# Kernel tuning notes

Hardware: AMD Instinct MI355X
Metric: run time of the kernel (lower is better)

Reference implementation:

```python
import jax, jax.numpy as jnp
import numpy as np

D_MODEL = 2048
NUM_Q_HEADS = 32
NUM_KV_HEADS = 8
HEAD_DIM = D_MODEL // NUM_Q_HEADS  # 64
NUM_GROUPS = NUM_Q_HEADS // NUM_KV_HEADS  # 4
SCALE = float(np.sqrt(HEAD_DIM))


def setup_inputs() -> dict:
    key = jax.random.key(0)
    ks = jax.random.split(key, 5)
    B, S = 2, 2048
    std = 1.0 / np.sqrt(D_MODEL)
    return {
        "x": jax.random.normal(ks[0], (B, S, D_MODEL), dtype=jnp.float32),
        "W_q": jax.random.normal(ks[1], (D_MODEL, NUM_Q_HEADS * HEAD_DIM), dtype=jnp.float32) * std,
        "W_k": jax.random.normal(ks[2], (D_MODEL, NUM_KV_HEADS * HEAD_DIM), dtype=jnp.float32) * std,
        "W_v": jax.random.normal(ks[3], (D_MODEL, NUM_KV_HEADS * HEAD_DIM), dtype=jnp.float32) * std,
        "W_o": jax.random.normal(ks[4], (D_MODEL, D_MODEL), dtype=jnp.float32) * std,
    }


def reference(x, W_q, W_k, W_v, W_o):
    B, S, _ = x.shape
    # projections; weights stored as (in, out) so y = x @ W
    Q = (x @ W_q).reshape(B, S, NUM_Q_HEADS, HEAD_DIM).transpose(0, 2, 1, 3)   # [B,Hq,S,d]
    K = (x @ W_k).reshape(B, S, NUM_KV_HEADS, HEAD_DIM).transpose(0, 2, 1, 3)  # [B,Hkv,S,d]
    V = (x @ W_v).reshape(B, S, NUM_KV_HEADS, HEAD_DIM).transpose(0, 2, 1, 3)
    # repeat_interleave KV heads across groups (faithful to the original)
    K = jnp.repeat(K, NUM_GROUPS, axis=1)  # [B,Hq,S,d]
    V = jnp.repeat(V, NUM_GROUPS, axis=1)
    scores = jnp.einsum("bhqd,bhkd->bhqk", Q, K) / SCALE  # [B,Hq,S,S]
    attn = jax.nn.softmax(scores, axis=-1)
    out = jnp.einsum("bhqk,bhkd->bhqd", attn, V)  # [B,Hq,S,d]
    out = out.transpose(0, 2, 1, 3).reshape(B, S, D_MODEL)
    return out @ W_o
```

## Files before the change

### kernel.cpp

```cpp
#include <hip/hip_runtime.h>
#include <hip/hip_bf16.h>

#define D_MODEL 2048
#define NQH 32
#define NKVH 8
#define HD 64
#define SEQ 2048
#define BATCH 2
#define MTOT (BATCH * SEQ)

typedef __attribute__((ext_vector_type(8))) short short8;
typedef __attribute__((ext_vector_type(4))) float floatx4;
typedef __attribute__((ext_vector_type(16))) float f32x16;

#define QSCALE 0.18033688011112042f

#if __has_builtin(__builtin_amdgcn_exp2f)
#define EXP2(x) __builtin_amdgcn_exp2f(x)
#else
#define EXP2(x) exp2f(x)
#endif

static __device__ inline unsigned cvtpk(float lo, float hi) {
  unsigned r;
  asm("v_cvt_pk_bf16_f32 %0, %1, %2" : "=v"(r) : "v"(lo), "v"(hi));
  return r;
}
#define PLSWAP(a, b) asm("v_permlane32_swap_b32 %0, %1" : "+v"(a), "+v"(b))

__device__ inline void gload_lds16(const __hip_bfloat16* g, short* lds) {
  __builtin_amdgcn_global_load_lds(
      (const __attribute__((address_space(1))) void*)g,
      (__attribute__((address_space(3))) void*)lds, 16, 0, 0);
}

__global__ __launch_bounds__(256) void convx_k(const float* __restrict__ x,
                                               __hip_bfloat16* __restrict__ xb,
                                               int n4) {
  int i = blockIdx.x * 256 + threadIdx.x;
  int stride = gridDim.x * 256;
  for (; i < n4; i += stride) {
    float4 v = reinterpret_cast<const float4*>(x)[i];
    union { __hip_bfloat16 h[4]; uint2 u; } cv;
    cv.h[0] = __float2bfloat16(v.x);
    cv.h[1] = __float2bfloat16(v.y);
    cv.h[2] = __float2bfloat16(v.z);
    cv.h[3] = __float2bfloat16(v.w);
    reinterpret_cast<uint2*>(xb)[i] = cv.u;
  }
}

__global__ __launch_bounds__(256) void transw_all_k(
    const float* __restrict__ Wq, const float* __restrict__ Wk,
    const float* __restrict__ Wv, const float* __restrict__ Wo,
    __hip_bfloat16* __restrict__ Wqt, __hip_bfloat16* __restrict__ Wkt,
    __hip_bfloat16* __restrict__ Wvt, __hip_bfloat16* __restrict__ Wot) {
  __shared__ float t[32][33];
  const int z = blockIdx.z;
  const int Nd = (z == 1 || z == 2) ? 512 : 2048;
  const int n0 = blockIdx.x * 32;
  if (n0 >= Nd) return;
  const float* W = (z == 0) ? Wq : (z == 1) ? Wk : (z == 2) ? Wv : Wo;
  __hip_bfloat16* Wt = (z == 0) ? Wqt : (z == 1) ? Wkt : (z == 2) ? Wvt : Wot;
  const int Kd = D_MODEL;
  const int k0 = blockIdx.y * 32;
  const int tx = threadIdx.x, ty = threadIdx.y;
#pragma unroll
  for (int j = 0; j < 32; j += 8)
    t[ty + j][tx] = W[(size_t)(k0 + ty + j) * Nd + n0 + tx];
  __syncthreads();
#pragma unroll
  for (int j = 0; j < 32; j += 8)
    Wt[(size_t)(n0 + ty + j) * Kd + k0 + tx] = __float2bfloat16(t[tx][ty + j]);
}

template <int MODE>
__global__ __launch_bounds__(512, 1) void gemm8p_k(
    const __hip_bfloat16* __restrict__ A,
    const __hip_bfloat16* __restrict__ B0,
    const __hip_bfloat16* __restrict__ B1,
    const __hip_bfloat16* __restrict__ B2,
    float* __restrict__ Cf,
    __hip_bfloat16* __restrict__ O0,
    __hip_bfloat16* __restrict__ O1,
    __hip_bfloat16* __restrict__ O2) {
  constexpr int Kd = D_MODEL;
  constexpr int NT = Kd / 64;
  constexpr int NB = (MODE == 0) ? 16 : 24;
  constexpr int NWG = 16 * NB;

  __shared__ short Asb[3][16384];
  __shared__ short Bsb[3][8192];

  const int bid = blockIdx.x;
  const int swz = (bid & 7) * (NWG / 8) + (bid >> 3);
  const int by = swz / NB, bx = swz % NB;
  const int m0 = by * 256, n0 = bx * 128;

  const __hip_bfloat16* Bt;
  if (MODE == 0) {
    Bt = B0 + (size_t)n0 * Kd;
  } else {
    if (n0 < 2048) Bt = B0 + (size_t)n0 * Kd;
    else if (n0 < 2560) Bt = B1 + (size_t)(n0 - 2048) * Kd;
    else Bt = B2 + (size_t)(n0 - 2560) * Kd;
  }
  const __hip_bfloat16* Ab = A + (size_t)m0 * Kd;

  const int tid = threadIdx.x, w = tid >> 6, l = tid & 63;
  const int wm = w >> 1, wn = w & 1;
  const int lc = l & 15, l4 = l >> 4;

  const int srow = w * 8 + (l >> 3);
  const int scc = (l & 7) ^ ((l >> 3) & 7);

#define STAGE_A(L, SB, KT) \
  gload_lds16(Ab + (size_t)((L)*64 + srow) * Kd + (KT) + scc * 8, &Asb[SB][(L)*4096 + w * 512])
#define STAGE_B(L, SB, KT) \
  gload_lds16(Bt + (size_t)((L)*64 + srow) * Kd + (KT) + scc * 8, &Bsb[SB][(L)*4096 + w * 512])

  floatx4 acc[4][4] = {};

  int cx[2];
#pragma unroll
  for (int kk = 0; kk < 2; ++kk) cx[kk] = (((kk * 4 + l4) ^ (lc & 7)) * 8);
  const int abase = (wm * 64 + lc) * 64;
  const int bbase = (wn * 64 + lc) * 64;

  STAGE_A(0, 0, 0); STAGE_A(1, 0, 0); STAGE_A(2, 0, 0); STAGE_A(3, 0, 0);
  STAGE_B(0, 0, 0); STAGE_B(1, 0, 0);
  STAGE_A(0, 1, 64); STAGE_A(1, 1, 64); STAGE_A(2, 1, 64); STAGE_A(3, 1, 64);
  STAGE_B(0, 1, 64); STAGE_B(1, 1, 64);
  asm volatile("s_waitcnt vmcnt(6)" ::: "memory");
  __builtin_amdgcn_s_barrier();

  short8 af[4], bfr[4];

  for (int t = 0; t < NT; ++t) {
    const int rb = t % 3, sb = (t + 2) % 3;
    const int ksrc = ((t + 2) % NT) * 64;
    const short* Ar = Asb[rb];
    const short* Br = Bsb[rb];

#pragma unroll
    for (int mi = 0; mi < 4; ++mi)
      af[mi] = *reinterpret_cast<const short8*>(&Ar[abase + mi * 1024 + cx[0]]);
#pragma unroll
    for (int ni = 0; ni < 4; ++ni)
      bfr[ni] = *reinterpret_cast<const short8*>(&Br[bbase + ni * 1024 + cx[0]]);

    STAGE_A(0, sb, ksrc); STAGE_A(1, sb, ksrc); STAGE_B(0, sb, ksrc);

    __builtin_amdgcn_s_barrier();
    asm volatile("s_waitcnt lgkmcnt(0)" ::: "memory");
    __builtin_amdgcn_sched_barrier(0);
    __builtin_amdgcn_s_setprio(1);
#pragma unroll
    for (int mi = 0; mi < 4; ++mi)
#pragma unroll
      for (int ni = 0; ni < 4; ++ni)
        acc[mi][ni] = __builtin_amdgcn_mfma_f32_16x16x32_bf16(
            af[mi], bfr[ni], acc[mi][ni], 0, 0, 0);
    __builtin_amdgcn_s_setprio(0);
    __builtin_amdgcn_s_barrier();

#pragma unroll
    for (int mi = 0; mi < 4; ++mi)
      af[mi] = *reinterpret_cast<const short8*>(&Ar[abase + mi * 1024 + cx[1]]);
#pragma unroll
    for (int ni = 0; ni < 4; ++ni)
      bfr[ni] = *reinterpret_cast<const short8*>(&Br[bbase + ni * 1024 + cx[1]]);

    STAGE_A(2, sb, ksrc); STAGE_A(3, sb, ksrc); STAGE_B(1, sb, ksrc);

    asm volatile("s_waitcnt vmcnt(6)" ::: "memory");
    __builtin_amdgcn_s_barrier();
    asm volatile("s_waitcnt lgkmcnt(0)" ::: "memory");
    __builtin_amdgcn_sched_barrier(0);
    __builtin_amdgcn_s_setprio(1);
#pragma unroll
    for (int mi = 0; mi < 4; ++mi)
#pragma unroll
      for (int ni = 0; ni < 4; ++ni)
        acc[mi][ni] = __builtin_amdgcn_mfma_f32_16x16x32_bf16(
            af[mi], bfr[ni], acc[mi][ni], 0, 0, 0);
    __builtin_amdgcn_s_setprio(0);
    __builtin_amdgcn_s_barrier();
  }
#undef STAGE_A
#undef STAGE_B

#pragma unroll
  for (int mi = 0; mi < 4; ++mi)
#pragma unroll
    for (int ni = 0; ni < 4; ++ni)
#pragma unroll
      for (int i = 0; i < 4; ++i) {
        int m = m0 + wm * 64 + mi * 16 + l4 * 4 + i;
        int ncol = n0 + wn * 64 + ni * 16 + lc;
        float v = acc[mi][ni][i];
        if (MODE == 0) {
          Cf[(size_t)m * 2048 + ncol] = v;
        } else {
          int bb = m >> 11, s = m & 2047;
          if (ncol < 2048) {
            int hh = ncol >> 6, dd = ncol & 63;
            O0[(((size_t)bb * NQH + hh) * SEQ + s) * HD + dd] = __float2bfloat16(v * QSCALE);
          } else if (ncol < 2560) {
            int c2 = ncol - 2048;
            int hh = c2 >> 6, dd = c2 & 63;
            O1[(((size_t)bb * NKVH + hh) * SEQ + s) * HD + dd] = __float2bfloat16(v);
          } else {
            int c2 = ncol - 2560;
            int hh = c2 >> 6, dd = c2 & 63;
            O2[(((size_t)bb * NKVH + hh) * HD + dd) * SEQ + s] = __float2bfloat16(v);
          }
        }
      }
}

__global__ __launch_bounds__(256, 4) void attn_k(const __hip_bfloat16* __restrict__ Qb,
                                                 const __hip_bfloat16* __restrict__ Kb,
                                                 const __hip_bfloat16* __restrict__ Vtb,
                                                 __hip_bfloat16* __restrict__ Ao) {
  __shared__ short Ks[2][64 * 64];
  __shared__ short Vs[2][64 * 64];
  __shared__ float Ls[4][32];

  const int bid = blockIdx.x;
  const int xcd = bid & 7, j = bid >> 3;
  const int g = xcd * 2 + (j >> 6), wv = j & 63;
  const int b = g >> 3, kh = g & 7;
  const int h = kh * 4 + (wv >> 4), qt = wv & 15;

  const int tid = threadIdx.x, w = tid >> 6, l = tid & 63;
  const int q5 = l & 31, hl = l >> 5;

  const __hip_bfloat16* Qp = Qb + (((size_t)b * NQH + h) * SEQ + qt * 128 + w * 32) * HD;
  const __hip_bfloat16* Kp = Kb + ((size_t)b * NKVH + kh) * SEQ * HD;
  const __hip_bfloat16* Vp = Vtb + ((size_t)b * NKVH + kh) * HD * SEQ;

  short8 qf[4];
#pragma unroll
  for (int ks = 0; ks < 4; ++ks)
    qf[ks] = *reinterpret_cast<const short8*>(Qp + (size_t)q5 * HD + ks * 16 + hl * 8);

  f32x16 acc0 = {}, acc1 = {};
  float lsum = 0.f;

  const int rg = l >> 3;
  const int cc = (l & 7) ^ (rg & 7);
  const __hip_bfloat16* sK = Kp + (size_t)(16 * w + rg) * HD + cc * 8;
  const __hip_bfloat16* sV = Vp + (size_t)(16 * w + rg) * SEQ + cc * 8;

  int fo[4];
#pragma unroll
  for (int jj = 0; jj < 4; ++jj)
    fo[jj] = q5 * 64 + (((jj * 2 + hl) ^ (q5 & 7)) * 8);

  gload_lds16(sK, &Ks[0][1024 * w]);
  gload_lds16(sK + 8 * HD, &Ks[0][1024 * w + 512]);
  gload_lds16(sV, &Vs[0][1024 * w]);
  gload_lds16(sV + 8 * (size_t)SEQ, &Vs[0][1024 * w + 512]);
  sK += 64 * HD;
  sV += 64;
  __syncthreads();

  for (int kb = 0; kb < SEQ / 64; ++kb) {
    const short* Kt = Ks[kb & 1];
    const short* Vt = Vs[kb & 1];

    if (kb + 1 < SEQ / 64) {
      short* Kn = Ks[(kb & 1) ^ 1];
      short* Vn = Vs[(kb & 1) ^ 1];
      gload_lds16(sK, &Kn[1024 * w]);
      gload_lds16(sK + 8 * HD, &Kn[1024 * w + 512]);
      gload_lds16(sV, &Vn[1024 * w]);
      gload_lds16(sV + 8 * (size_t)SEQ, &Vn[1024 * w + 512]);
      sK += 64 * HD;
      sV += 64;
    }

    short8 kf0[4], kf1[4];
#pragma unroll
    for (int ks = 0; ks < 4; ++ks) {
      kf0[ks] = *reinterpret_cast<const short8*>(&Kt[fo[ks]]);
      kf1[ks] = *reinterpret_cast<const short8*>(&Kt[fo[ks] + 2048]);
    }
    f32x16 st0 = {}, st1 = {};
    __builtin_amdgcn_s_setprio(1);
#pragma unroll
    for (int ks = 0; ks < 4; ++ks) {
      st0 = __builtin_amdgcn_mfma_f32_32x32x16_bf16(kf0[ks], qf[ks], st0, 0, 0, 0);
      st1 = __builtin_amdgcn_mfma_f32_32x32x16_bf16(kf1[ks], qf[ks], st1, 0, 0, 0);
    }
    __builtin_amdgcn_s_setprio(0);

    float ps = 0.f;
    unsigned u0[8], u1[8];
#pragma unroll
    for (int jj = 0; jj < 8; ++jj) {
      float e0 = EXP2(st0[2 * jj]), e1 = EXP2(st0[2 * jj + 1]);
      float f0 = EXP2(st1[2 * jj]), f1 = EXP2(st1[2 * jj + 1]);
      ps += (e0 + e1) + (f0 + f1);
      u0[jj] = cvtpk(e0, e1);
      u1[jj] = cvtpk(f0, f1);
    }
    lsum += ps;

    short8 vf0[4], vf1[4];
#pragma unroll
    for (int t = 0; t < 4; ++t) {
      vf0[t] = *reinterpret_cast<const short8*>(&Vt[fo[t]]);
      vf1[t] = *reinterpret_cast<const short8*>(&Vt[fo[t] + 2048]);
    }

    PLSWAP(u0[0], u0[2]); PLSWAP(u0[1], u0[3]);
    PLSWAP(u0[4], u0[6]); PLSWAP(u0[5], u0[7]);
    PLSWAP(u1[0], u1[2]); PLSWAP(u1[1], u1[3]);
    PLSWAP(u1[4], u1[6]); PLSWAP(u1[5], u1[7]);

    __builtin_amdgcn_s_setprio(1);
#pragma unroll
    for (int t = 0; t < 4; ++t) {
      union { unsigned w4[4]; short8 s8; } pa;
      pa.w4[0] = (t >> 1 ? u1 : u0)[(t & 1) * 4 + 0];
      pa.w4[1] = (t >> 1 ? u1 : u0)[(t & 1) * 4 + 1];
      pa.w4[2] = (t >> 1 ? u1 : u0)[(t & 1) * 4 + 2];
      pa.w4[3] = (t >> 1 ? u1 : u0)[(t & 1) * 4 + 3];
      acc0 = __builtin_amdgcn_mfma_f32_32x32x16_bf16(pa.s8, vf0[t], acc0, 0, 0, 0);
      acc1 = __builtin_amdgcn_mfma_f32_32x32x16_bf16(pa.s8, vf1[t], acc1, 0, 0, 0);
    }
    __builtin_amdgcn_s_setprio(0);
    __syncthreads();
  }

  {
    float v = lsum;
    v += __shfl_xor(v, 32);
    if (l < 32) Ls[w][l] = v;
  }
  __syncthreads();

  const size_t obase = (size_t)b * SEQ + qt * 128 + w * 32;
  float inv[16];
#pragma unroll
  for (int r = 0; r < 16; ++r)
    inv[r] = 1.0f / Ls[w][(r & 3) + 8 * (r >> 2) + 4 * hl];
#pragma unroll
  for (int r = 0; r < 16; ++r) {
    int q = (r & 3) + 8 * (r >> 2) + 4 * hl;
    Ao[(obase + q) * D_MODEL + h * HD + q5] = __float2bfloat16(acc0[r] * inv[r]);
    Ao[(obase + q) * D_MODEL + h * HD + 32 + q5] = __float2bfloat16(acc1[r] * inv[r]);
  }
}

extern "C" void kernel_launch(void* const* d_in, const int* in_sizes, int n_in,
                              void* d_out, int out_size, void* d_ws, size_t ws_size,
                              hipStream_t stream) {
  const float* x  = (const float*)d_in[0];
  const float* Wq = (const float*)d_in[1];
  const float* Wk = (const float*)d_in[2];
  const float* Wv = (const float*)d_in[3];
  const float* Wo = (const float*)d_in[4];
  float* out = (float*)d_out;

  __hip_bfloat16* p = (__hip_bfloat16*)d_ws;
  __hip_bfloat16* xb  = p;
  __hip_bfloat16* Wqt = xb  + (size_t)MTOT * D_MODEL;
  __hip_bfloat16* Wkt = Wqt + (size_t)D_MODEL * D_MODEL;
  __hip_bfloat16* Wvt = Wkt + (size_t)512 * D_MODEL;
  __hip_bfloat16* Wot = Wvt + (size_t)512 * D_MODEL;
  __hip_bfloat16* Qb  = Wot + (size_t)D_MODEL * D_MODEL;
  __hip_bfloat16* Kb  = Qb  + (size_t)MTOT * D_MODEL;
  __hip_bfloat16* Vtb = Kb  + (size_t)BATCH * NKVH * SEQ * HD;
  __hip_bfloat16* Ab  = Vtb + (size_t)BATCH * NKVH * SEQ * HD;

  convx_k<<<2048, 256, 0, stream>>>(x, xb, MTOT * D_MODEL / 4);
  transw_all_k<<<dim3(64, 64, 4), dim3(32, 8), 0, stream>>>(Wq, Wk, Wv, Wo,
                                                            Wqt, Wkt, Wvt, Wot);

  gemm8p_k<1><<<dim3(16 * 24), 512, 0, stream>>>(xb, Wqt, Wkt, Wvt,
                                                 nullptr, Qb, Kb, Vtb);
  attn_k<<<dim3(1024), 256, 0, stream>>>(Qb, Kb, Vtb, Ab);
  gemm8p_k<0><<<dim3(16 * 16), 512, 0, stream>>>(Ab, Wot, nullptr, nullptr,
                                                 out, nullptr, nullptr, nullptr);
}
```

Measured before the change: 222.3 us.

## Widen QKV GEMM tile to 256x192 and pad attention LDS with register-staged prefetch

The fused QKV projection gets its own kernel with a 256x192 tile, so 256 workgroups exactly cover the 3072-column output instead of 384 with 128-wide tiles. It uses a simpler double-buffered pipeline with a full vmcnt wait each iteration. The attention kernel replaces direct global-to-LDS loads and XOR swizzling with register-staged prefetch into row-padded (68-element) LDS tiles, written after the PV MFMAs. The aim is a single wave of GEMM workgroups and fewer bank conflicts, at the cost of more registers and possibly less latency hiding.

```diff
diff --git a/kernel.cpp b/kernel.cpp
--- a/kernel.cpp
+++ b/kernel.cpp
@@ -74,19 +74,130 @@
     Wt[(size_t)(n0 + ty + j) * Kd + k0 + tx] = __float2bfloat16(t[tx][ty + j]);
 }
 
-template <int MODE>
-__global__ __launch_bounds__(512, 1) void gemm8p_k(
+__global__ __launch_bounds__(512, 1) void gemmqkv_k(
     const __hip_bfloat16* __restrict__ A,
     const __hip_bfloat16* __restrict__ B0,
     const __hip_bfloat16* __restrict__ B1,
     const __hip_bfloat16* __restrict__ B2,
-    float* __restrict__ Cf,
     __hip_bfloat16* __restrict__ O0,
     __hip_bfloat16* __restrict__ O1,
     __hip_bfloat16* __restrict__ O2) {
   constexpr int Kd = D_MODEL;
   constexpr int NT = Kd / 64;
-  constexpr int NB = (MODE == 0) ? 16 : 24;
+
+  __shared__ short Asb[2][16384];
+  __shared__ short Bsb[2][12288];
+
+  const int bid = blockIdx.x;
+  const int swz = (bid & 7) * 32 + (bid >> 3);
+  const int by = swz >> 4, bx = swz & 15;
+  const int m0 = by * 256, n0 = bx * 192;
+
+  const __hip_bfloat16* Ab = A + (size_t)m0 * Kd;
+
+  const __hip_bfloat16* bp[3];
+#pragma unroll
+  for (int L = 0; L < 3; ++L) {
+    int nr = n0 + L * 64;
+    bp[L] = (nr < 2048) ? B0 + (size_t)nr * Kd
+          : (nr < 2560) ? B1 + (size_t)(nr - 2048) * Kd
+                        : B2 + (size_t)(nr - 2560) * Kd;
+  }
+
+  const int tid = threadIdx.x, w = tid >> 6, l = tid & 63;
+  const int wm = w >> 1, wn = w & 1;
+  const int lc = l & 15, l4 = l >> 4;
+
+  const int srow = w * 8 + (l >> 3);
+  const int scc = (l & 7) ^ ((l >> 3) & 7);
+
+#define STAGE_A(L, SB, KT) \
+  gload_lds16(Ab + (size_t)((L)*64 + srow) * Kd + (KT) + scc * 8, &Asb[SB][(L)*4096 + w * 512])
+#define STAGE_B(L, SB, KT) \
+  gload_lds16(bp[L] + (size_t)srow * Kd + (KT) + scc * 8, &Bsb[SB][(L)*4096 + w * 512])
+
+  floatx4 acc[4][6] = {};
+
+  int cx[2];
+#pragma unroll
+  for (int kk = 0; kk < 2; ++kk) cx[kk] = (((kk * 4 + l4) ^ (lc & 7)) * 8);
+  const int abase = (wm * 64 + lc) * 64;
+  const int bbase = (wn * 96 + lc) * 64;
+
+  STAGE_A(0, 0, 0); STAGE_A(1, 0, 0); STAGE_A(2, 0, 0); STAGE_A(3, 0, 0);
+  STAGE_B(0, 0, 0); STAGE_B(1, 0, 0); STAGE_B(2, 0, 0);
+  asm volatile("s_waitcnt vmcnt(0)" ::: "memory");
+  __builtin_amdgcn_s_barrier();
+
+  short8 af[4], bfr[6];
+
+  for (int t = 0; t < NT; ++t) {
+    const int rb = t & 1, sb = rb ^ 1;
+    const short* Ar = Asb[rb];
+    const short* Br = Bsb[rb];
+
+    if (t + 1 < NT) {
+      const int kt = (t + 1) * 64;
+      STAGE_A(0, sb, kt); STAGE_A(1, sb, kt); STAGE_A(2, sb, kt); STAGE_A(3, sb, kt);
+      STAGE_B(0, sb, kt); STAGE_B(1, sb, kt); STAGE_B(2, sb, kt);
+    }
+
+#pragma unroll
+    for (int kk = 0; kk < 2; ++kk) {
+#pragma unroll
+      for (int mi = 0; mi < 4; ++mi)
+        af[mi] = *reinterpret_cast<const short8*>(&Ar[abase + mi * 1024 + cx[kk]]);
+#pragma unroll
+      for (int ni = 0; ni < 6; ++ni)
+        bfr[ni] = *reinterpret_cast<const short8*>(&Br[bbase + ni * 1024 + cx[kk]]);
+      __builtin_amdgcn_s_setprio(1);
+#pragma unroll
+      for (int mi = 0; mi < 4; ++mi)
+#pragma unroll
+        for (int ni = 0; ni < 6; ++ni)
+          acc[mi][ni] = __builtin_amdgcn_mfma_f32_16x16x32_bf16(
+              af[mi], bfr[ni], acc[mi][ni], 0, 0, 0);
+      __builtin_amdgcn_s_setprio(0);
+    }
+
+    asm volatile("s_waitcnt vmcnt(0)" ::: "memory");
+    __builtin_amdgcn_s_barrier();
+  }
+#undef STAGE_A
+#undef STAGE_B
+
+#pragma unroll
+  for (int mi = 0; mi < 4; ++mi)
+#pragma unroll
+    for (int ni = 0; ni < 6; ++ni)
+#pragma unroll
+      for (int i = 0; i < 4; ++i) {
+        int m = m0 + wm * 64 + mi * 16 + l4 * 4 + i;
+        int ncol = n0 + wn * 96 + ni * 16 + lc;
+        float v = acc[mi][ni][i];
+        int bb = m >> 11, s = m & 2047;
+        if (ncol < 2048) {
+          int hh = ncol >> 6, dd = ncol & 63;
+          O0[(((size_t)bb * NQH + hh) * SEQ + s) * HD + dd] = __float2bfloat16(v * QSCALE);
+        } else if (ncol < 2560) {
+          int c2 = ncol - 2048;
+          int hh = c2 >> 6, dd = c2 & 63;
+          O1[(((size_t)bb * NKVH + hh) * SEQ + s) * HD + dd] = __float2bfloat16(v);
+        } else {
+          int c2 = ncol - 2560;
+          int hh = c2 >> 6, dd = c2 & 63;
+          O2[(((size_t)bb * NKVH + hh) * HD + dd) * SEQ + s] = __float2bfloat16(v);
+        }
+      }
+}
+
+__global__ __launch_bounds__(512, 1) void gemmo_k(
+    const __hip_bfloat16* __restrict__ A,
+    const __hip_bfloat16* __restrict__ B0,
+    float* __restrict__ Cf) {
+  constexpr int Kd = D_MODEL;
+  constexpr int NT = Kd / 64;
+  constexpr int NB = 16;
   constexpr int NWG = 16 * NB;
 
   __shared__ short Asb[3][16384];
@@ -97,14 +208,7 @@
   const int by = swz / NB, bx = swz % NB;
   const int m0 = by * 256, n0 = bx * 128;
 
-  const __hip_bfloat16* Bt;
-  if (MODE == 0) {
-    Bt = B0 + (size_t)n0 * Kd;
-  } else {
-    if (n0 < 2048) Bt = B0 + (size_t)n0 * Kd;
-    else if (n0 < 2560) Bt = B1 + (size_t)(n0 - 2048) * Kd;
-    else Bt = B2 + (size_t)(n0 - 2560) * Kd;
-  }
+  const __hip_bfloat16* Bt = B0 + (size_t)n0 * Kd;
   const __hip_bfloat16* Ab = A + (size_t)m0 * Kd;
 
   const int tid = threadIdx.x, w = tid >> 6, l = tid & 63;
@@ -198,24 +302,7 @@
       for (int i = 0; i < 4; ++i) {
         int m = m0 + wm * 64 + mi * 16 + l4 * 4 + i;
         int ncol = n0 + wn * 64 + ni * 16 + lc;
-        float v = acc[mi][ni][i];
-        if (MODE == 0) {
-          Cf[(size_t)m * 2048 + ncol] = v;
-        } else {
-          int bb = m >> 11, s = m & 2047;
-          if (ncol < 2048) {
-            int hh = ncol >> 6, dd = ncol & 63;
-            O0[(((size_t)bb * NQH + hh) * SEQ + s) * HD + dd] = __float2bfloat16(v * QSCALE);
-          } else if (ncol < 2560) {
-            int c2 = ncol - 2048;
-            int hh = c2 >> 6, dd = c2 & 63;
-            O1[(((size_t)bb * NKVH + hh) * SEQ + s) * HD + dd] = __float2bfloat16(v);
-          } else {
-            int c2 = ncol - 2560;
-            int hh = c2 >> 6, dd = c2 & 63;
-            O2[(((size_t)bb * NKVH + hh) * HD + dd) * SEQ + s] = __float2bfloat16(v);
-          }
-        }
+        Cf[(size_t)m * 2048 + ncol] = acc[mi][ni][i];
       }
 }
 
@@ -223,8 +310,8 @@
                                                  const __hip_bfloat16* __restrict__ Kb,
                                                  const __hip_bfloat16* __restrict__ Vtb,
                                                  __hip_bfloat16* __restrict__ Ao) {
-  __shared__ short Ks[2][64 * 64];
-  __shared__ short Vs[2][64 * 64];
+  __shared__ short Ks[2][64 * 68];
+  __shared__ short Vs[2][64 * 68];
   __shared__ float Ls[4][32];
 
   const int bid = blockIdx.x;
@@ -248,44 +335,49 @@
   f32x16 acc0 = {}, acc1 = {};
   float lsum = 0.f;
 
-  const int rg = l >> 3;
-  const int cc = (l & 7) ^ (rg & 7);
-  const __hip_bfloat16* sK = Kp + (size_t)(16 * w + rg) * HD + cc * 8;
-  const __hip_bfloat16* sV = Vp + (size_t)(16 * w + rg) * SEQ + cc * 8;
+  const int rg = l >> 3, ch = l & 7;
+  const __hip_bfloat16* sK = Kp + (size_t)(16 * w + rg) * HD + ch * 8;
+  const __hip_bfloat16* sV = Vp + (size_t)(16 * w + rg) * SEQ + ch * 8;
+  const int wo0 = (16 * w + rg) * 68 + ch * 8;
+  const int wo1 = wo0 + 8 * 68;
 
   int fo[4];
 #pragma unroll
   for (int jj = 0; jj < 4; ++jj)
-    fo[jj] = q5 * 64 + (((jj * 2 + hl) ^ (q5 & 7)) * 8);
-
-  gload_lds16(sK, &Ks[0][1024 * w]);
-  gload_lds16(sK + 8 * HD, &Ks[0][1024 * w + 512]);
-  gload_lds16(sV, &Vs[0][1024 * w]);
-  gload_lds16(sV + 8 * (size_t)SEQ, &Vs[0][1024 * w + 512]);
-  sK += 64 * HD;
-  sV += 64;
+    fo[jj] = q5 * 68 + (jj * 2 + hl) * 8;
+
+  {
+    short8 k0 = *reinterpret_cast<const short8*>(sK);
+    short8 k1 = *reinterpret_cast<const short8*>(sK + 8 * HD);
+    short8 v0 = *reinterpret_cast<const short8*>(sV);
+    short8 v1 = *reinterpret_cast<const short8*>(sV + 8 * (size_t)SEQ);
+    sK += 64 * HD; sV += 64;
+    *reinterpret_cast<short8*>(&Ks[0][wo0]) = k0;
+    *reinterpret_cast<short8*>(&Ks[0][wo1]) = k1;
+    *reinterpret_cast<short8*>(&Vs[0][wo0]) = v0;
+    *reinterpret_cast<short8*>(&Vs[0][wo1]) = v1;
+  }
   __syncthreads();
 
   for (int kb = 0; kb < SEQ / 64; ++kb) {
     const short* Kt = Ks[kb & 1];
     const short* Vt = Vs[kb & 1];
-
-    if (kb + 1 < SEQ / 64) {
-      short* Kn = Ks[(kb & 1) ^ 1];
-      short* Vn = Vs[(kb & 1) ^ 1];
-      gload_lds16(sK, &Kn[1024 * w]);
-      gload_lds16(sK + 8 * HD, &Kn[1024 * w + 512]);
-      gload_lds16(sV, &Vn[1024 * w]);
-      gload_lds16(sV + 8 * (size_t)SEQ, &Vn[1024 * w + 512]);
-      sK += 64 * HD;
-      sV += 64;
+    const bool pf = (kb + 1 < SEQ / 64);
+
+    short8 nk0, nk1, nv0, nv1;
+    if (pf) {
+      nk0 = *reinterpret_cast<const short8*>(sK);
+      nk1 = *reinterpret_cast<const short8*>(sK + 8 * HD);
+      nv0 = *reinterpret_cast<const short8*>(sV);
+      nv1 = *reinterpret_cast<const short8*>(sV + 8 * (size_t)SEQ);
+      sK += 64 * HD; sV += 64;
     }
 
     short8 kf0[4], kf1[4];
 #pragma unroll
     for (int ks = 0; ks < 4; ++ks) {
       kf0[ks] = *reinterpret_cast<const short8*>(&Kt[fo[ks]]);
-      kf1[ks] = *reinterpret_cast<const short8*>(&Kt[fo[ks] + 2048]);
+      kf1[ks] = *reinterpret_cast<const short8*>(&Kt[fo[ks] + 2176]);
     }
     f32x16 st0 = {}, st1 = {};
     __builtin_amdgcn_s_setprio(1);
@@ -312,7 +404,7 @@
 #pragma unroll
     for (int t = 0; t < 4; ++t) {
       vf0[t] = *reinterpret_cast<const short8*>(&Vt[fo[t]]);
-      vf1[t] = *reinterpret_cast<const short8*>(&Vt[fo[t] + 2048]);
+      vf1[t] = *reinterpret_cast<const short8*>(&Vt[fo[t] + 2176]);
     }
 
     PLSWAP(u0[0], u0[2]); PLSWAP(u0[1], u0[3]);
@@ -332,6 +424,15 @@
       acc1 = __builtin_amdgcn_mfma_f32_32x32x16_bf16(pa.s8, vf1[t], acc1, 0, 0, 0);
     }
     __builtin_amdgcn_s_setprio(0);
+
+    if (pf) {
+      short* Kn = Ks[(kb & 1) ^ 1];
+      short* Vn = Vs[(kb & 1) ^ 1];
+      *reinterpret_cast<short8*>(&Kn[wo0]) = nk0;
+      *reinterpret_cast<short8*>(&Kn[wo1]) = nk1;
+      *reinterpret_cast<short8*>(&Vn[wo0]) = nv0;
+      *reinterpret_cast<short8*>(&Vn[wo1]) = nv1;
+    }
     __syncthreads();
   }
 
@@ -380,9 +481,7 @@
   transw_all_k<<<dim3(64, 64, 4), dim3(32, 8), 0, stream>>>(Wq, Wk, Wv, Wo,
                                                             Wqt, Wkt, Wvt, Wot);
 
-  gemm8p_k<1><<<dim3(16 * 24), 512, 0, stream>>>(xb, Wqt, Wkt, Wvt,
-                                                 nullptr, Qb, Kb, Vtb);
+  gemmqkv_k<<<dim3(256), 512, 0, stream>>>(xb, Wqt, Wkt, Wvt, Qb, Kb, Vtb);
   attn_k<<<dim3(1024), 256, 0, stream>>>(Qb, Kb, Vtb, Ab);
-  gemm8p_k<0><<<dim3(16 * 16), 512, 0, stream>>>(Ab, Wot, nullptr, nullptr,
-                                                 out, nullptr, nullptr, nullptr);
-}
+  gemmo_k<<<dim3(256), 512, 0, stream>>>(Ab, Wot, out);
+}
```

Result: slower. 396.2 us (+78.2%).
